# Performance work log

Measured on AMD Instinct MI355X. Metric: run time of the kernel, lower is better.

The kernel has to match this reference:

```python
import jax, jax.numpy as jnp
from jax import lax
import numpy as np

NUM_GRIDS = (40, 36, 24, 16, 12)
B, C = 4, 256
SMPL_OUT, CATE_OUT = 157, 1  # 24*6 pose + 10 shape + 3 cam; num_classes-1
SIZES = ((200, 200), (100, 100), (50, 50), (25, 25), (13, 13))


def setup_inputs():
    key = jax.random.key(0)
    ks = jax.random.split(key, 16)
    inp = {}
    for i, (h, w) in enumerate(SIZES):
        inp['feat%d' % i] = jax.random.normal(ks[i], (B, C, h, w), jnp.float32)
    def W(k, shape):
        return jax.random.normal(k, shape, jnp.float32) * 0.02
    inp['smpl_w0'] = W(ks[5], (C, C + 2, 3, 3)); inp['smpl_b0'] = jnp.zeros((C,), jnp.float32)
    inp['smpl_w'] = W(ks[6], (3, C, C, 3, 3)); inp['smpl_b'] = jnp.zeros((3, C), jnp.float32)
    inp['cate_w0'] = W(ks[7], (C, C, 3, 3)); inp['cate_b0'] = jnp.zeros((C,), jnp.float32)
    inp['cate_w'] = W(ks[8], (3, C, C, 3, 3)); inp['cate_b'] = jnp.zeros((3, C), jnp.float32)
    inp['cate_head_w'] = W(ks[9], (CATE_OUT, C, 3, 3)); inp['cate_head_b'] = jnp.zeros((CATE_OUT,), jnp.float32)
    inp['smpl_head_w'] = W(ks[10], (SMPL_OUT, C, 1, 1)); inp['smpl_head_b'] = jnp.zeros((SMPL_OUT,), jnp.float32)
    inp['smpl_init'] = W(ks[11], (SMPL_OUT,))  # stands in for init_contrep/shape/cam buffer
    return inp


def conv2d(x, w, b, pad):
    y = lax.conv_general_dilated(x, w, (1, 1), [(pad, pad), (pad, pad)],
                                 dimension_numbers=('NCHW', 'OIHW', 'NCHW'))
    return y + b[None, :, None, None]


def resize_ac(x, oh, ow):
    # bilinear resize, align_corners=True (matches F.interpolate(..., align_corners=True))
    H, W = x.shape[-2], x.shape[-1]
    ys = jnp.linspace(0.0, H - 1.0, oh)
    xs = jnp.linspace(0.0, W - 1.0, ow)
    y0 = jnp.floor(ys).astype(jnp.int32); y1 = jnp.minimum(y0 + 1, H - 1)
    x0 = jnp.floor(xs).astype(jnp.int32); x1 = jnp.minimum(x0 + 1, W - 1)
    wy = (ys - y0)[:, None]; wx = xs - x0
    r0, r1 = x[..., y0, :], x[..., y1, :]
    top = r0[..., x0] * (1 - wx) + r0[..., x1] * wx
    bot = r1[..., x0] * (1 - wx) + r1[..., x1] * wx
    return top * (1 - wy) + bot * wy


def points_nms(heat):
    # max_pool2d(kernel=2, stride=1, pad=1) -> (H+1, W+1); compare on [:-1, :-1]
    hmax = lax.reduce_window(heat, -jnp.inf, lax.max, (1, 1, 2, 2), (1, 1, 1, 1),
                             [(0, 0), (0, 0), (1, 1), (1, 1)])[:, :, :-1, :-1]
    return heat * (hmax == heat).astype(heat.dtype)


def _forward(feats, p):
    # split_feats: downsample P2 by 0.5, upsample P6 to P5 size (both align_corners bilinear)
    f0 = resize_ac(feats[0], feats[0].shape[-2] // 2, feats[0].shape[-1] // 2)
    f4 = resize_ac(feats[4], feats[3].shape[-2], feats[3].shape[-1])
    new_feats = (f0, feats[1], feats[2], feats[3], f4)
    smpl_outs, cate_outs = [], []
    for idx, x in enumerate(new_feats):
        g = NUM_GRIDS[idx]
        b, _, h, w = x.shape
        xr = jnp.linspace(-1.0, 1.0, w); yr = jnp.linspace(-1.0, 1.0, h)
        yy, xx = jnp.meshgrid(yr, xr, indexing='ij')
        coord = jnp.broadcast_to(jnp.stack([xx, yy])[None], (b, 2, h, w))  # CoordConv
        smpl_feat = resize_ac(jnp.concatenate([x, coord], axis=1), g, g)
        cate_feat = resize_ac(x, g, g)
        smpl_feat = jax.nn.relu(conv2d(smpl_feat, p['smpl_w0'], p['smpl_b0'], 1))
        cate_feat = jax.nn.relu(conv2d(cate_feat, p['cate_w0'], p['cate_b0'], 1))
        for i in range(3):  # remaining stacked convs (weights shared across levels)
            smpl_feat = jax.nn.relu(conv2d(smpl_feat, p['smpl_w'][i], p['smpl_b'][i], 1))
            cate_feat = jax.nn.relu(conv2d(cate_feat, p['cate_w'][i], p['cate_b'][i], 1))
        cate_pred = conv2d(cate_feat, p['cate_head_w'], p['cate_head_b'], 1)
        smpl_pred = conv2d(smpl_feat, p['smpl_head_w'], p['smpl_head_b'], 0) \
                    + p['smpl_init'][None, :, None, None]
        # eval=True branch: points-NMS on sigmoid heatmap, NHWC permute
        cate_pred = points_nms(jax.nn.sigmoid(cate_pred)).transpose(0, 2, 3, 1)
        smpl_pred = smpl_pred.transpose(0, 2, 3, 1)
        smpl_outs.append(smpl_pred); cate_outs.append(cate_pred)
    return tuple(smpl_outs) + tuple(cate_outs)


def reference(feat0, feat1, feat2, feat3, feat4, smpl_w0, smpl_b0, smpl_w, smpl_b,
              cate_w0, cate_b0, cate_w, cate_b, cate_head_w, cate_head_b,
              smpl_head_w, smpl_head_b, smpl_init):
    p = dict(smpl_w0=smpl_w0, smpl_b0=smpl_b0, smpl_w=smpl_w, smpl_b=smpl_b,
             cate_w0=cate_w0, cate_b0=cate_b0, cate_w=cate_w, cate_b=cate_b,
             cate_head_w=cate_head_w, cate_head_b=cate_head_b,
             smpl_head_w=smpl_head_w, smpl_head_b=smpl_head_b, smpl_init=smpl_init)
    return _forward((feat0, feat1, feat2, feat3, feat4), p)
```

## Files before the change

kernel.cpp:

```cpp
#include <hip/hip_runtime.h>
#include <math.h>
#include <stdint.h>

#define NLEV 5
#define PPT 17616
#define HPX 320

typedef __attribute__((ext_vector_type(8))) __bf16 bf16x8;
typedef __attribute__((ext_vector_type(4))) float f32x4;
typedef unsigned int u32;
typedef unsigned short u16;

#define MFMA16 __builtin_amdgcn_mfma_f32_16x16x32_bf16

__device__ __forceinline__ u32 f2bf(float f) {
  u32 u = __builtin_bit_cast(u32, f);
  return (u + 0x7FFFu + ((u >> 16) & 1u)) >> 16;
}
__device__ __forceinline__ u32 packSplit(float v) {
  u32 hi = f2bf(v);
  float fhi = __builtin_bit_cast(float, hi << 16);
  u32 lo = f2bf(v - fhi);
  return hi | (lo << 16);
}
__device__ __forceinline__ float unpackSum(u32 w) {
  return __builtin_bit_cast(float, w << 16) +
         __builtin_bit_cast(float, w & 0xFFFF0000u);
}
__device__ __forceinline__ void splitPerm(const uint4& a, const uint4& b, uint4& hq,
                                          uint4& lq) {
  hq.x = __builtin_amdgcn_perm(a.y, a.x, 0x05040100u);
  hq.y = __builtin_amdgcn_perm(a.w, a.z, 0x05040100u);
  hq.z = __builtin_amdgcn_perm(b.y, b.x, 0x05040100u);
  hq.w = __builtin_amdgcn_perm(b.w, b.z, 0x05040100u);
  lq.x = __builtin_amdgcn_perm(a.y, a.x, 0x07060302u);
  lq.y = __builtin_amdgcn_perm(a.w, a.z, 0x07060302u);
  lq.z = __builtin_amdgcn_perm(b.y, b.x, 0x07060302u);
  lq.w = __builtin_amdgcn_perm(b.w, b.z, 0x07060302u);
}


struct PrepDesc {
  const float* src[9];
  int Cin[9];
  int Cout[9];
  int CB[9];
  int TAPS[9];
  int nCoT[9];
  int dstOff[9];
};

__global__ __launch_bounds__(256) void prep_weights(PrepDesc pd, u16* __restrict__ wHi,
                                                    u16* __restrict__ wLo) {
  int cfg = blockIdx.y;
  int CB = pd.CB[cfg];
  int TAPS = pd.TAPS[cfg];
  int KS = CB * TAPS;
  int total = KS * 2048 * pd.nCoT[cfg];
  int didx = blockIdx.x * 256 + threadIdx.x;
  if (didx >= total) return;
  int j = didx & 7;
  int lane = (didx >> 3) & 63;
  int wco = (didx >> 9) & 1;
  int f = (didx >> 10) & 1;
  int rest = didx >> 11;
  int ks = rest % KS;
  int coT = rest / KS;
  int cb = ks / TAPS;
  int tap = ks - cb * TAPS;
  int ci = cb * 32 + ((lane >> 4) << 3) + j;
  int co = coT * 64 + wco * 32 + f * 16 + (lane & 15);
  float v = 0.f;
  if (ci < pd.Cin[cfg] && co < pd.Cout[cfg])
    v = pd.src[cfg][((size_t)co * pd.Cin[cfg] + ci) * TAPS + tap];
  u32 hi = f2bf(v);
  float fhi = __builtin_bit_cast(float, hi << 16);
  u32 lo = f2bf(v - fhi);
  wHi[pd.dstOff[cfg] + didx] = (u16)hi;
  wLo[pd.dstOff[cfg] + didx] = (u16)lo;
}

struct ZeroDesc {
  int padOff[NLEV];
  int g[NLEV];
};

__global__ __launch_bounds__(256) void halo_zero(u32* __restrict__ base, ZeroDesc zd) {
  int px = blockIdx.x * 256 + threadIdx.x;
  if (px >= PPT) return;
  int l = 0;
#pragma unroll
  for (int i = 1; i < NLEV; i++)
    if (px >= zd.padOff[i]) l = i;
  int g = zd.g[l], gp2 = g + 2, hp2 = gp2 * gp2;
  int local = px - zd.padOff[l];
  int b = local / hp2;
  int rem = local - b * hp2;
  int yy = rem / gp2, xx = rem - yy * gp2;
  if (yy >= 1 && yy <= g && xx >= 1 && xx <= g) return;
  int r = blockIdx.y;
  uint4 z = {0u, 0u, 0u, 0u};
  u32* p = base + ((size_t)r * PPT + px) * 8;
  *(uint4*)p = z;
  *(uint4*)(p + 4) = z;
}

struct BuildDesc {
  const float* src[NLEV];
  int H[NLEV];
  int mid[NLEV];
  int P[NLEV];
  int g[NLEV];
  int padOff[NLEV];
};

__device__ __forceinline__ float bsample(const float* __restrict__ pl, int H, int W,
                                         float fy, float fx) {
  int y0 = (int)floorf(fy);
  int y1 = min(y0 + 1, H - 1);
  float wy = fy - (float)y0;
  int x0 = (int)floorf(fx);
  int x1 = min(x0 + 1, W - 1);
  float wx = fx - (float)x0;
  const float* r0 = pl + (size_t)y0 * W;
  const float* r1 = pl + (size_t)y1 * W;
  float top = r0[x0] * (1.f - wx) + r0[x1] * wx;
  float bot = r1[x0] * (1.f - wx) + r1[x1] * wx;
  return top * (1.f - wy) + bot * wy;
}

__global__ __launch_bounds__(256) void build_all(BuildDesc bd, u32* __restrict__ dst) {
  int l = blockIdx.y;
  int P = bd.P[l];
  int g = bd.g[l];
  int total = 258 * P;
  int idx = blockIdx.x * 256 + threadIdx.x;
  if (idx >= total) return;
  int c = idx / P;
  int p = idx - c * P;
  int gg = g * g;
  int b = p / gg;
  int pr = p - b * gg;
  int i = pr / g;
  int j = pr - i * g;
  float val;
  if (c >= 256) {
    int tt = (c == 256) ? j : i;
    val = -1.f + 2.f * (float)tt / (float)(g - 1);
  } else {
    int H = bd.H[l], W = bd.H[l];
    int mid = bd.mid[l];
    const float* pl = bd.src[l] + ((size_t)b * 256 + c) * H * W;
    if (!mid) {
      float fy = (float)i * (float)(H - 1) / (float)(g - 1);
      float fx = (float)j * (float)(W - 1) / (float)(g - 1);
      val = bsample(pl, H, W, fy, fx);
    } else {
      int midh = mid, midw = mid;
      float fym = (float)i * (float)(midh - 1) / (float)(g - 1);
      float fxm = (float)j * (float)(midw - 1) / (float)(g - 1);
      int y0 = (int)floorf(fym);
      int y1 = min(y0 + 1, midh - 1);
      float wy = fym - (float)y0;
      int x0 = (int)floorf(fxm);
      int x1 = min(x0 + 1, midw - 1);
      float wx = fxm - (float)x0;
      float sy0 = (float)y0 * (float)(H - 1) / (float)(midh - 1);
      float sy1 = (float)y1 * (float)(H - 1) / (float)(midh - 1);
      float sx0 = (float)x0 * (float)(W - 1) / (float)(midw - 1);
      float sx1 = (float)x1 * (float)(W - 1) / (float)(midw - 1);
      float v00 = bsample(pl, H, W, sy0, sx0);
      float v01 = bsample(pl, H, W, sy0, sx1);
      float v10 = bsample(pl, H, W, sy1, sx0);
      float v11 = bsample(pl, H, W, sy1, sx1);
      float top = v00 * (1.f - wx) + v01 * wx;
      float bot = v10 * (1.f - wx) + v11 * wx;
      val = top * (1.f - wy) + bot * wy;
    }
  }
  int gp2 = g + 2;
  int hpos = bd.padOff[l] + b * gp2 * gp2 + (i + 1) * gp2 + (j + 1);
  dst[((size_t)(c >> 3) * PPT + hpos) * 8 + (c & 7)] = packSplit(val);
}

struct ConvDesc {
  int tS[NLEV + 1];
  int padOff[NLEV];
  int g[NLEV];
  int P[NLEV];
};

__global__ __launch_bounds__(256) void conv_mfma(
    const u32* __restrict__ inS, const u32* __restrict__ inC,
    const u16* __restrict__ wHiB, const u16* __restrict__ wLoB, int wOffS,
    int wOffC, const float* __restrict__ bS, const float* __restrict__ bC,
    u32* __restrict__ outS, u32* __restrict__ outC, ConvDesc d, int CBS, int CBC) {
  const int bid = blockIdx.x;
  const int xcd = bid & 7;
  const int i6 = bid >> 3;
  const int tower = i6 & 1;
  const int coT = (i6 >> 1) & 3;
  const int tile = xcd + (i6 >> 3) * 8;
  if (tile >= d.tS[NLEV]) return;

  const u32* __restrict__ actIn = tower ? inC : inS;
  u32* __restrict__ actOut = tower ? outC : outS;
  const u16* __restrict__ wH = wHiB + (tower ? wOffC : wOffS);
  const u16* __restrict__ wL = wLoB + (tower ? wOffC : wOffS);
  const float* __restrict__ bias = tower ? bC : bS;
  const int CB = tower ? CBC : CBS;
  const int KS = CB * 9;

  int l = 0;
#pragma unroll
  for (int i = 1; i < NLEV; i++)
    if (tile >= d.tS[i]) l = i;
  const int g = d.g[l];
  const int gp2 = g + 2, hp2 = gp2 * gp2, gg = g * g;
  const int padOff = d.padOff[l];
  const int Pl = d.P[l];
  const int ptile = (tile - d.tS[l]) * 128;

  const int t = threadIdx.x;
  const int lane = t & 63;
  const int wv = t >> 6;
  const int wco = wv & 1, wp = wv >> 1;
  const int kb = lane >> 4;
  const int sgr = wv;
  const int spx = lane;

  int h0;
  {
    int b0 = ptile / gg, pr0 = ptile - b0 * gg;
    int y0 = pr0 / g, x0 = pr0 - y0 * g;
    h0 = padOff + b0 * hp2 + (y0 + 1) * gp2 + (x0 + 1) - gp2 - 1;
  }

  int hRel[4], ob[4];
  bool vst[4];
#pragma unroll
  for (int fi = 0; fi < 4; fi++) {
    int pb = ptile + wp * 64 + fi * 16;
    vst[fi] = pb < Pl;
    int pf = pb + (lane & 15);
    if (pf >= Pl) pf = Pl - 1;
    int b = pf / gg, pr = pf - b * gg;
    int y = pr / g, x = pr - y * g;
    int h = padOff + b * hp2 + (y + 1) * gp2 + (x + 1);
    hRel[fi] = h - h0;
    ob[fi] = h;
  }

  __shared__ u32 halo[4 * 2 * HPX * 4];

  f32x4 acc[2][4];
#pragma unroll
  for (int c = 0; c < 2; c++)
#pragma unroll
    for (int fi = 0; fi < 4; fi++) acc[c][fi] = (f32x4){0.f, 0.f, 0.f, 0.f};

  const size_t wbase =
      (size_t)coT * KS * 2048 + (size_t)wco * 512 + (size_t)lane * 8;
  bf16x8 ah0 = *(const bf16x8*)(wH + wbase);
  bf16x8 ah1 = *(const bf16x8*)(wH + wbase + 1024);
  bf16x8 al0 = *(const bf16x8*)(wL + wbase);
  bf16x8 al1 = *(const bf16x8*)(wL + wbase + 1024);

  for (int cb = 0; cb < CB; ++cb) {
    __syncthreads();
    {
      const int gr = cb * 4 + sgr;
      const u32* srcp = actIn + ((size_t)gr * PPT + h0) * 8;
      u32* dhi = halo + sgr * (2 * HPX * 4);
      u32* dlo = dhi + HPX * 4;
#pragma unroll
      for (int i = 0; i < 5; i++) {
        int px = i * 64 + spx;
        uint4 a = *(const uint4*)(srcp + (size_t)px * 8);
        uint4 b2 = *(const uint4*)(srcp + (size_t)px * 8 + 4);
        uint4 hq, lq;
        splitPerm(a, b2, hq, lq);
        *(uint4*)(dhi + px * 4) = hq;
        *(uint4*)(dlo + px * 4) = lq;
      }
    }
    __syncthreads();

#pragma unroll
    for (int tap = 0; tap < 9; ++tap) {
      const int ks = cb * 9 + tap;
      bf16x8 ah0n, ah1n, al0n, al1n;
      const bool have = (ks + 1) < KS;
      if (have) {
        size_t wo = wbase + (size_t)(ks + 1) * 2048;
        ah0n = *(const bf16x8*)(wH + wo);
        ah1n = *(const bf16x8*)(wH + wo + 1024);
        al0n = *(const bf16x8*)(wL + wo);
        al1n = *(const bf16x8*)(wL + wo + 1024);
      }
      const int toff = (tap / 3 - 1) * gp2 + (tap % 3) - 1;
      const u32* kbase = halo + kb * (2 * HPX * 4);
#pragma unroll
      for (int fi = 0; fi < 4; fi++) {
        const u32* p0 = kbase + (hRel[fi] + toff) * 4;
        bf16x8 bh = __builtin_bit_cast(bf16x8, *(const uint4*)p0);
        bf16x8 bl = __builtin_bit_cast(bf16x8, *(const uint4*)(p0 + HPX * 4));
        acc[0][fi] = MFMA16(ah0, bh, acc[0][fi], 0, 0, 0);
        acc[0][fi] = MFMA16(ah0, bl, acc[0][fi], 0, 0, 0);
        acc[0][fi] = MFMA16(al0, bh, acc[0][fi], 0, 0, 0);
        acc[1][fi] = MFMA16(ah1, bh, acc[1][fi], 0, 0, 0);
        acc[1][fi] = MFMA16(ah1, bl, acc[1][fi], 0, 0, 0);
        acc[1][fi] = MFMA16(al1, bh, acc[1][fi], 0, 0, 0);
      }
      if (have) {
        ah0 = ah0n;
        ah1 = ah1n;
        al0 = al0n;
        al1 = al1n;
      }
    }
  }

  const int coBase = coT * 64 + wco * 32 + ((lane >> 4) << 2);
  float4 bA = *(const float4*)(bias + coBase);
  float4 bB = *(const float4*)(bias + coBase + 16);
  const size_t rowA = (size_t)(coBase >> 3) * PPT;
  const size_t rowB = (size_t)((coBase + 16) >> 3) * PPT;
  const int sub = coBase & 7;
#pragma unroll
  for (int fi = 0; fi < 4; fi++) {
    if (!vst[fi]) continue;
    uint4 s;
    s.x = packSplit(fmaxf(acc[0][fi][0] + bA.x, 0.f));
    s.y = packSplit(fmaxf(acc[0][fi][1] + bA.y, 0.f));
    s.z = packSplit(fmaxf(acc[0][fi][2] + bA.z, 0.f));
    s.w = packSplit(fmaxf(acc[0][fi][3] + bA.w, 0.f));
    *(uint4*)(actOut + (rowA + ob[fi]) * 8 + sub) = s;
    s.x = packSplit(fmaxf(acc[1][fi][0] + bB.x, 0.f));
    s.y = packSplit(fmaxf(acc[1][fi][1] + bB.y, 0.f));
    s.z = packSplit(fmaxf(acc[1][fi][2] + bB.z, 0.f));
    s.w = packSplit(fmaxf(acc[1][fi][3] + bB.w, 0.f));
    *(uint4*)(actOut + (rowB + ob[fi]) * 8 + sub) = s;
  }
}

struct HeadDesc {
  int tS64[NLEV + 1];
  int padOff[NLEV];
  int g[NLEV];
  int outOff[NLEV];
};

__global__ __launch_bounds__(256) void head1x1(
    const u32* __restrict__ actIn, const u16* __restrict__ wH,
    const u16* __restrict__ wL, const float* __restrict__ bias,
    const float* __restrict__ bias2, float* __restrict__ outB, HeadDesc d) {
  const int bx = blockIdx.x;
  const int coT = blockIdx.y;
  int l = 0;
#pragma unroll
  for (int i = 1; i < NLEV; i++)
    if (bx >= d.tS64[i]) l = i;
  const int g = d.g[l], gp2 = g + 2, hp2 = gp2 * gp2, gg = g * g;
  const int ptile = (bx - d.tS64[l]) * 64;
  const int t = threadIdx.x, lane = t & 63, wv = t >> 6;
  const int wco = wv & 1, wp = wv >> 1, kb = lane >> 4;

  int hp[2], pF[2];
#pragma unroll
  for (int fi = 0; fi < 2; fi++) {
    int pf = ptile + wp * 32 + fi * 16 + (lane & 15);
    pF[fi] = pf;
    int b = pf / gg, pr = pf - b * gg, y = pr / g, x = pr - y * g;
    hp[fi] = d.padOff[l] + b * hp2 + (y + 1) * gp2 + (x + 1);
  }
  f32x4 acc[2][2];
#pragma unroll
  for (int c = 0; c < 2; c++)
#pragma unroll
    for (int fi = 0; fi < 2; fi++) acc[c][fi] = (f32x4){0.f, 0.f, 0.f, 0.f};

  const size_t wbase = (size_t)coT * 8 * 2048 + (size_t)wco * 512 + (size_t)lane * 8;
  for (int cb = 0; cb < 8; ++cb) {
    size_t wo = wbase + (size_t)cb * 2048;
    bf16x8 ah0 = *(const bf16x8*)(wH + wo);
    bf16x8 ah1 = *(const bf16x8*)(wH + wo + 1024);
    bf16x8 al0 = *(const bf16x8*)(wL + wo);
    bf16x8 al1 = *(const bf16x8*)(wL + wo + 1024);
    const int gr = cb * 4 + kb;
#pragma unroll
    for (int fi = 0; fi < 2; fi++) {
      const u32* bp = actIn + ((size_t)gr * PPT + hp[fi]) * 8;
      uint4 a = *(const uint4*)bp;
      uint4 b2 = *(const uint4*)(bp + 4);
      uint4 hq, lq;
      splitPerm(a, b2, hq, lq);
      bf16x8 bh = __builtin_bit_cast(bf16x8, hq);
      bf16x8 bl = __builtin_bit_cast(bf16x8, lq);
      acc[0][fi] = MFMA16(ah0, bh, acc[0][fi], 0, 0, 0);
      acc[0][fi] = MFMA16(ah0, bl, acc[0][fi], 0, 0, 0);
      acc[0][fi] = MFMA16(al0, bh, acc[0][fi], 0, 0, 0);
      acc[1][fi] = MFMA16(ah1, bh, acc[1][fi], 0, 0, 0);
      acc[1][fi] = MFMA16(ah1, bl, acc[1][fi], 0, 0, 0);
      acc[1][fi] = MFMA16(al1, bh, acc[1][fi], 0, 0, 0);
    }
  }
  const int coBase = coT * 64 + wco * 32 + ((lane >> 4) << 2);
#pragma unroll
  for (int c = 0; c < 2; c++)
#pragma unroll
    for (int fi = 0; fi < 2; fi++)
#pragma unroll
      for (int i = 0; i < 4; i++) {
        int co = coBase + c * 16 + i;
        if (co < 157)
          outB[d.outOff[l] + (size_t)pF[fi] * 157 + co] =
              acc[c][fi][i] + bias[co] + bias2[co];
      }
}

struct CHDesc {
  int tS64[NLEV + 1];
  int padOff[NLEV];
  int g[NLEV];
  int outOff[NLEV];
};

__global__ __launch_bounds__(256) void cate_head_all(
    const u32* __restrict__ actIn, const float* __restrict__ w,
    const float* __restrict__ bias, float* __restrict__ heat, CHDesc d) {
  int tile = blockIdx.x;
  int l = 0;
#pragma unroll
  for (int i = 1; i < NLEV; i++)
    if (tile >= d.tS64[i]) l = i;
  const int g = d.g[l];
  const int gp2 = g + 2, hp2 = gp2 * gp2, gg = g * g;
  const int t = threadIdx.x;
  const int ps = t & 63;
  const int cw = t >> 6;
  const int ptile = (tile - d.tS64[l]) * 64;
  int p = ptile + ps;
  int b = p / gg, pr = p - b * gg, y = pr / g, x = pr - y * g;
  const int hbase = d.padOff[l] + b * hp2 + (y + 1) * gp2 + (x + 1);

  __shared__ float ws[32][9][8];
  for (int i = t; i < 2304; i += 256) {
    int ci = i / 9, tap = i - ci * 9;
    ws[ci >> 3][tap][ci & 7] = w[i];
  }
  __syncthreads();

  float s = 0.f;
  for (int gr = cw; gr < 32; gr += 4) {
    const u32* bp = actIn + ((size_t)gr * PPT + hbase) * 8;
#pragma unroll
    for (int tap = 0; tap < 9; tap++) {
      const int toff = (tap / 3 - 1) * gp2 + (tap % 3) - 1;
      uint4 q0 = *(const uint4*)(bp + (ptrdiff_t)toff * 8);
      uint4 q1 = *(const uint4*)(bp + (ptrdiff_t)toff * 8 + 4);
      const float* wp = ws[gr][tap];
      s += unpackSum(q0.x) * wp[0] + unpackSum(q0.y) * wp[1] +
           unpackSum(q0.z) * wp[2] + unpackSum(q0.w) * wp[3] +
           unpackSum(q1.x) * wp[4] + unpackSum(q1.y) * wp[5] +
           unpackSum(q1.z) * wp[6] + unpackSum(q1.w) * wp[7];
    }
  }
  __shared__ float red[4][64];
  red[cw][ps] = s;
  __syncthreads();
  if (cw == 0) {
    float tot = bias[0] + red[0][ps] + red[1][ps] + red[2][ps] + red[3][ps];
    heat[d.outOff[l] + p] = 1.f / (1.f + expf(-tot));
  }
}

struct SmallDesc {
  int P[NLEV];
  int g[NLEV];
  int inOff[NLEV];
  int outOff[NLEV];
};

__global__ void nms_all(const float* __restrict__ heat, float* __restrict__ out,
                        SmallDesc d) {
  int l = blockIdx.y;
  int P = d.P[l], g = d.g[l];
  int gg = g * g;
  int p = blockIdx.x * 256 + threadIdx.x;
  if (p >= P) return;
  int pr = p % gg;
  int y = pr / g;
  int x = pr - y * g;
  const float* hb = heat + d.inOff[l];
  float c = hb[p], m = c;
  if (y > 0) {
    m = fmaxf(m, hb[p - g]);
    if (x > 0) m = fmaxf(m, hb[p - g - 1]);
  }
  if (x > 0) m = fmaxf(m, hb[p - 1]);
  out[d.outOff[l] + p] = (m == c) ? c : 0.f;
}

extern "C" void kernel_launch(void* const* d_in, const int* in_sizes, int n_in,
                              void* d_out, int out_size, void* d_ws, size_t ws_size,
                              hipStream_t stream) {
  const float* feat[5];
  for (int i = 0; i < 5; i++) feat[i] = (const float*)d_in[i];
  const float* smpl_w0 = (const float*)d_in[5];
  const float* smpl_b0 = (const float*)d_in[6];
  const float* smpl_w = (const float*)d_in[7];
  const float* smpl_b = (const float*)d_in[8];
  const float* cate_w0 = (const float*)d_in[9];
  const float* cate_b0 = (const float*)d_in[10];
  const float* cate_w = (const float*)d_in[11];
  const float* cate_b = (const float*)d_in[12];
  const float* cate_head_w = (const float*)d_in[13];
  const float* cate_head_b = (const float*)d_in[14];
  const float* smpl_head_w = (const float*)d_in[15];
  const float* smpl_head_b = (const float*)d_in[16];
  const float* smpl_init = (const float*)d_in[17];
  float* out = (float*)d_out;

  static const int GR[5] = {40, 36, 24, 16, 12};
  static const int SH[5] = {200, 100, 50, 25, 13};
  static const int MIDW[5] = {100, 0, 0, 0, 25};

  int P[5], cumP[6], tS64[6], tS128[6], padOff[5];
  cumP[0] = 0;
  tS64[0] = 0;
  tS128[0] = 0;
  int po = 0;
  for (int l = 0; l < 5; l++) {
    P[l] = 4 * GR[l] * GR[l];
    cumP[l + 1] = cumP[l] + P[l];
    tS64[l + 1] = tS64[l] + P[l] / 64;
    tS128[l + 1] = tS128[l] + (P[l] + 127) / 128;
    padOff[l] = po;
    po += 4 * (GR[l] + 2) * (GR[l] + 2);
  }

  int smpl_off[5], cate_off[5];
  {
    int off = 0;
    for (int l = 0; l < 5; l++) {
      smpl_off[l] = off;
      off += P[l] * 157;
    }
    for (int l = 0; l < 5; l++) {
      cate_off[l] = off;
      off += P[l];
    }
  }

  u32* bufA = (u32*)d_ws;
  u32* bufBs = bufA + (size_t)36 * PPT * 8;
  u32* bufCs = bufBs + (size_t)32 * PPT * 8;
  u32* bufBc = bufCs + (size_t)32 * PPT * 8;
  u32* bufCc = bufBc + (size_t)32 * PPT * 8;
  float* heat = (float*)(bufCc + (size_t)32 * PPT * 8);
  u16* wHi = (u16*)(heat + 15488);

  PrepDesc pd;
  const size_t LSTR = (size_t)256 * 256 * 9;
  pd.src[0] = smpl_w0;
  pd.src[1] = smpl_w;
  pd.src[2] = smpl_w + LSTR;
  pd.src[3] = smpl_w + 2 * LSTR;
  pd.src[4] = cate_w0;
  pd.src[5] = cate_w;
  pd.src[6] = cate_w + LSTR;
  pd.src[7] = cate_w + 2 * LSTR;
  pd.src[8] = smpl_head_w;
  for (int i = 0; i < 9; i++) {
    pd.Cin[i] = 256;
    pd.Cout[i] = 256;
    pd.CB[i] = 8;
    pd.TAPS[i] = 9;
    pd.nCoT[i] = 4;
  }
  pd.Cin[0] = 258;
  pd.CB[0] = 9;
  pd.Cout[8] = 157;
  pd.TAPS[8] = 1;
  pd.nCoT[8] = 3;
  size_t WTOT = 0;
  for (int i = 0; i < 9; i++) {
    pd.dstOff[i] = (int)WTOT;
    WTOT += (size_t)pd.CB[i] * pd.TAPS[i] * 2048 * pd.nCoT[i];
  }
  u16* wLo = wHi + WTOT;

  hipMemsetAsync(bufA, 0, (size_t)36 * PPT * 32, stream);
  ZeroDesc zd;
  for (int l = 0; l < 5; l++) {
    zd.padOff[l] = padOff[l];
    zd.g[l] = GR[l];
  }
  hipLaunchKernelGGL(halo_zero, dim3((PPT + 255) / 256, 128), dim3(256), 0, stream,
                     bufBs, zd);

  hipLaunchKernelGGL(prep_weights, dim3(2592, 9), dim3(256), 0, stream, pd, wHi, wLo);

  BuildDesc bd;
  for (int l = 0; l < 5; l++) {
    bd.src[l] = feat[l];
    bd.H[l] = SH[l];
    bd.mid[l] = MIDW[l];
    bd.P[l] = P[l];
    bd.g[l] = GR[l];
    bd.padOff[l] = padOff[l];
  }
  hipLaunchKernelGGL(build_all, dim3((258 * P[0] + 255) / 256, 5), dim3(256), 0,
                     stream, bd, bufA);

  ConvDesc cd;
  HeadDesc hd;
  CHDesc chd;
  SmallDesc nd;
  for (int i = 0; i <= 5; i++) {
    cd.tS[i] = tS128[i];
    hd.tS64[i] = tS64[i];
    chd.tS64[i] = tS64[i];
  }
  for (int l = 0; l < 5; l++) {
    cd.padOff[l] = padOff[l];
    cd.g[l] = GR[l];
    cd.P[l] = P[l];
    hd.padOff[l] = padOff[l];
    hd.g[l] = GR[l];
    hd.outOff[l] = smpl_off[l];
    chd.padOff[l] = padOff[l];
    chd.g[l] = GR[l];
    chd.outOff[l] = cumP[l];
    nd.P[l] = P[l];
    nd.g[l] = GR[l];
    nd.inOff[l] = cumP[l];
    nd.outOff[l] = cate_off[l];
  }

  const int NT64 = tS64[5];
  const int CGRID = 8 * 128;
  hipLaunchKernelGGL(conv_mfma, dim3(CGRID), dim3(256), 0, stream, bufA, bufA, wHi,
                     wLo, pd.dstOff[0], pd.dstOff[4], smpl_b0, cate_b0, bufBs, bufBc,
                     cd, 9, 8);
  hipLaunchKernelGGL(conv_mfma, dim3(CGRID), dim3(256), 0, stream, bufBs, bufBc, wHi,
                     wLo, pd.dstOff[1], pd.dstOff[5], smpl_b + 0, cate_b + 0, bufCs,
                     bufCc, cd, 8, 8);
  hipLaunchKernelGGL(conv_mfma, dim3(CGRID), dim3(256), 0, stream, bufCs, bufCc, wHi,
                     wLo, pd.dstOff[2], pd.dstOff[6], smpl_b + 256, cate_b + 256,
                     bufBs, bufBc, cd, 8, 8);
  hipLaunchKernelGGL(conv_mfma, dim3(CGRID), dim3(256), 0, stream, bufBs, bufBc, wHi,
                     wLo, pd.dstOff[3], pd.dstOff[7], smpl_b + 512, cate_b + 512,
                     bufCs, bufCc, cd, 8, 8);
  hipLaunchKernelGGL(head1x1, dim3(NT64, 3), dim3(256), 0, stream, bufCs,
                     wHi + pd.dstOff[8], wLo + pd.dstOff[8], smpl_head_b, smpl_init,
                     out, hd);
  hipLaunchKernelGGL(cate_head_all, dim3(NT64), dim3(256), 0, stream, bufCc,
                     cate_head_w, cate_head_b, heat, chd);
  hipLaunchKernelGGL(nms_all, dim3((P[0] + 255) / 256, 5), dim3(256), 0, stream, heat,
                     out, nd);
  (void)in_sizes;
  (void)n_in;
  (void)out_size;
  (void)ws_size;
}
```

Before: 528.5 us.

## Store activations as split hi/lo planes and double-buffer halo via async LDS loads

Activations were stored as interleaved packed hi/lo bf16 words that each conv block split with perm instructions while staging into shared memory. They are now stored as separate hi and lo planes, so staging can use global_load_lds direct-to-LDS copies into a double-buffered halo. The next channel block is prefetched while MFMAs run on the current one, which removes the perm work and one barrier per iteration. In exchange shared memory use doubles, which may reduce occupancy, and the epilogue now issues narrower 8-byte stores.

```diff
diff --git a/kernel.cpp b/kernel.cpp
--- a/kernel.cpp
+++ b/kernel.cpp
@@ -17,26 +17,12 @@
   u32 u = __builtin_bit_cast(u32, f);
   return (u + 0x7FFFu + ((u >> 16) & 1u)) >> 16;
 }
-__device__ __forceinline__ u32 packSplit(float v) {
-  u32 hi = f2bf(v);
-  float fhi = __builtin_bit_cast(float, hi << 16);
-  u32 lo = f2bf(v - fhi);
-  return hi | (lo << 16);
-}
-__device__ __forceinline__ float unpackSum(u32 w) {
-  return __builtin_bit_cast(float, w << 16) +
-         __builtin_bit_cast(float, w & 0xFFFF0000u);
-}
-__device__ __forceinline__ void splitPerm(const uint4& a, const uint4& b, uint4& hq,
-                                          uint4& lq) {
-  hq.x = __builtin_amdgcn_perm(a.y, a.x, 0x05040100u);
-  hq.y = __builtin_amdgcn_perm(a.w, a.z, 0x05040100u);
-  hq.z = __builtin_amdgcn_perm(b.y, b.x, 0x05040100u);
-  hq.w = __builtin_amdgcn_perm(b.w, b.z, 0x05040100u);
-  lq.x = __builtin_amdgcn_perm(a.y, a.x, 0x07060302u);
-  lq.y = __builtin_amdgcn_perm(a.w, a.z, 0x07060302u);
-  lq.z = __builtin_amdgcn_perm(b.y, b.x, 0x07060302u);
-  lq.w = __builtin_amdgcn_perm(b.w, b.z, 0x07060302u);
+__device__ __forceinline__ void split2(float v, u32& hi, u32& lo) {
+  hi = f2bf(v);
+  lo = f2bf(v - __builtin_bit_cast(float, hi << 16));
+}
+__device__ __forceinline__ float bf2f(u32 bits16) {
+  return __builtin_bit_cast(float, bits16 << 16);
 }
 
 
@@ -73,9 +59,8 @@
   float v = 0.f;
   if (ci < pd.Cin[cfg] && co < pd.Cout[cfg])
     v = pd.src[cfg][((size_t)co * pd.Cin[cfg] + ci) * TAPS + tap];
-  u32 hi = f2bf(v);
-  float fhi = __builtin_bit_cast(float, hi << 16);
-  u32 lo = f2bf(v - fhi);
+  u32 hi, lo;
+  split2(v, hi, lo);
   wHi[pd.dstOff[cfg] + didx] = (u16)hi;
   wLo[pd.dstOff[cfg] + didx] = (u16)lo;
 }
@@ -85,7 +70,7 @@
   int g[NLEV];
 };
 
-__global__ __launch_bounds__(256) void halo_zero(u32* __restrict__ base, ZeroDesc zd) {
+__global__ __launch_bounds__(256) void halo_zero(u16* __restrict__ base, ZeroDesc zd) {
   int px = blockIdx.x * 256 + threadIdx.x;
   if (px >= PPT) return;
   int l = 0;
@@ -100,9 +85,7 @@
   if (yy >= 1 && yy <= g && xx >= 1 && xx <= g) return;
   int r = blockIdx.y;
   uint4 z = {0u, 0u, 0u, 0u};
-  u32* p = base + ((size_t)r * PPT + px) * 8;
-  *(uint4*)p = z;
-  *(uint4*)(p + 4) = z;
+  *(uint4*)(base + ((size_t)r * PPT + px) * 8) = z;
 }
 
 struct BuildDesc {
@@ -129,7 +112,7 @@
   return top * (1.f - wy) + bot * wy;
 }
 
-__global__ __launch_bounds__(256) void build_all(BuildDesc bd, u32* __restrict__ dst) {
+__global__ __launch_bounds__(256) void build_all(BuildDesc bd, u16* __restrict__ dst) {
   int l = blockIdx.y;
   int P = bd.P[l];
   int g = bd.g[l];
@@ -180,7 +163,11 @@
   }
   int gp2 = g + 2;
   int hpos = bd.padOff[l] + b * gp2 * gp2 + (i + 1) * gp2 + (j + 1);
-  dst[((size_t)(c >> 3) * PPT + hpos) * 8 + (c & 7)] = packSplit(val);
+  u32 hi, lo;
+  split2(val, hi, lo);
+  size_t base = ((size_t)(c >> 3) * PPT + hpos) * 8 + (c & 7);
+  dst[base] = (u16)hi;
+  dst[(size_t)36 * PPT * 8 + base] = (u16)lo;
 }
 
 struct ConvDesc {
@@ -191,10 +178,10 @@
 };
 
 __global__ __launch_bounds__(256) void conv_mfma(
-    const u32* __restrict__ inS, const u32* __restrict__ inC,
+    const u16* __restrict__ inS, const u16* __restrict__ inC, int inRows,
     const u16* __restrict__ wHiB, const u16* __restrict__ wLoB, int wOffS,
     int wOffC, const float* __restrict__ bS, const float* __restrict__ bC,
-    u32* __restrict__ outS, u32* __restrict__ outC, ConvDesc d, int CBS, int CBC) {
+    u16* __restrict__ outS, u16* __restrict__ outC, ConvDesc d, int CBS, int CBC) {
   const int bid = blockIdx.x;
   const int xcd = bid & 7;
   const int i6 = bid >> 3;
@@ -203,8 +190,10 @@
   const int tile = xcd + (i6 >> 3) * 8;
   if (tile >= d.tS[NLEV]) return;
 
-  const u32* __restrict__ actIn = tower ? inC : inS;
-  u32* __restrict__ actOut = tower ? outC : outS;
+  const u16* __restrict__ inHi = tower ? inC : inS;
+  const u16* __restrict__ inLo = inHi + (size_t)inRows * PPT * 8;
+  u16* __restrict__ outHi = tower ? outC : outS;
+  u16* __restrict__ outLo = outHi + (size_t)32 * PPT * 8;
   const u16* __restrict__ wH = wHiB + (tower ? wOffC : wOffS);
   const u16* __restrict__ wL = wLoB + (tower ? wOffC : wOffS);
   const float* __restrict__ bias = tower ? bC : bS;
@@ -227,7 +216,6 @@
   const int wco = wv & 1, wp = wv >> 1;
   const int kb = lane >> 4;
   const int sgr = wv;
-  const int spx = lane;
 
   int h0;
   {
@@ -251,7 +239,7 @@
     ob[fi] = h;
   }
 
-  __shared__ u32 halo[4 * 2 * HPX * 4];
+  __shared__ u16 halo[2 * 4 * 2 * HPX * 8];
 
   f32x4 acc[2][4];
 #pragma unroll
@@ -266,25 +254,31 @@
   bf16x8 al0 = *(const bf16x8*)(wL + wbase);
   bf16x8 al1 = *(const bf16x8*)(wL + wbase + 1024);
 
+#define STAGE(dbuf, cbn)                                                          \
+  {                                                                               \
+    const int gr_ = (cbn)*4 + sgr;                                                \
+    const u16* ghi_ = inHi + ((size_t)gr_ * PPT + h0) * 8;                        \
+    const u16* glo_ = inLo + ((size_t)gr_ * PPT + h0) * 8;                        \
+    u16* lb_ = halo + (size_t)(((dbuf)*4 + sgr) * 2) * (HPX * 8);                 \
+    _Pragma("unroll") for (int i_ = 0; i_ < 5; i_++) {                            \
+      __builtin_amdgcn_global_load_lds(                                           \
+          (const __attribute__((address_space(1))) void*)(ghi_ +                  \
+                                                          (size_t)(i_ * 64 + lane) * 8), \
+          (__attribute__((address_space(3))) void*)(lb_ + i_ * 64 * 8), 16, 0, 0);\
+      __builtin_amdgcn_global_load_lds(                                           \
+          (const __attribute__((address_space(1))) void*)(glo_ +                  \
+                                                          (size_t)(i_ * 64 + lane) * 8), \
+          (__attribute__((address_space(3))) void*)(lb_ + HPX * 8 + i_ * 64 * 8), \
+          16, 0, 0);                                                              \
+    }                                                                             \
+  }
+
+  STAGE(0, 0);
+
   for (int cb = 0; cb < CB; ++cb) {
+    const int cur = cb & 1;
     __syncthreads();
-    {
-      const int gr = cb * 4 + sgr;
-      const u32* srcp = actIn + ((size_t)gr * PPT + h0) * 8;
-      u32* dhi = halo + sgr * (2 * HPX * 4);
-      u32* dlo = dhi + HPX * 4;
-#pragma unroll
-      for (int i = 0; i < 5; i++) {
-        int px = i * 64 + spx;
-        uint4 a = *(const uint4*)(srcp + (size_t)px * 8);
-        uint4 b2 = *(const uint4*)(srcp + (size_t)px * 8 + 4);
-        uint4 hq, lq;
-        splitPerm(a, b2, hq, lq);
-        *(uint4*)(dhi + px * 4) = hq;
-        *(uint4*)(dlo + px * 4) = lq;
-      }
-    }
-    __syncthreads();
+    if (cb + 1 < CB) STAGE(cur ^ 1, cb + 1);
 
 #pragma unroll
     for (int tap = 0; tap < 9; ++tap) {
@@ -299,12 +293,12 @@
         al1n = *(const bf16x8*)(wL + wo + 1024);
       }
       const int toff = (tap / 3 - 1) * gp2 + (tap % 3) - 1;
-      const u32* kbase = halo + kb * (2 * HPX * 4);
+      const u16* kbase = halo + (size_t)((cur * 4 + kb) * 2) * (HPX * 8);
 #pragma unroll
       for (int fi = 0; fi < 4; fi++) {
-        const u32* p0 = kbase + (hRel[fi] + toff) * 4;
-        bf16x8 bh = __builtin_bit_cast(bf16x8, *(const uint4*)p0);
-        bf16x8 bl = __builtin_bit_cast(bf16x8, *(const uint4*)(p0 + HPX * 4));
+        const u16* p0 = kbase + (hRel[fi] + toff) * 8;
+        bf16x8 bh = *(const bf16x8*)p0;
+        bf16x8 bl = *(const bf16x8*)(p0 + HPX * 8);
         acc[0][fi] = MFMA16(ah0, bh, acc[0][fi], 0, 0, 0);
         acc[0][fi] = MFMA16(ah0, bl, acc[0][fi], 0, 0, 0);
         acc[0][fi] = MFMA16(al0, bh, acc[0][fi], 0, 0, 0);
@@ -320,27 +314,38 @@
       }
     }
   }
+#undef STAGE
 
   const int coBase = coT * 64 + wco * 32 + ((lane >> 4) << 2);
-  float4 bA = *(const float4*)(bias + coBase);
-  float4 bB = *(const float4*)(bias + coBase + 16);
+  float bAv[4], bBv[4];
+#pragma unroll
+  for (int i = 0; i < 4; i++) {
+    bAv[i] = bias[coBase + i];
+    bBv[i] = bias[coBase + 16 + i];
+  }
   const size_t rowA = (size_t)(coBase >> 3) * PPT;
   const size_t rowB = (size_t)((coBase + 16) >> 3) * PPT;
   const int sub = coBase & 7;
 #pragma unroll
   for (int fi = 0; fi < 4; fi++) {
     if (!vst[fi]) continue;
-    uint4 s;
-    s.x = packSplit(fmaxf(acc[0][fi][0] + bA.x, 0.f));
-    s.y = packSplit(fmaxf(acc[0][fi][1] + bA.y, 0.f));
-    s.z = packSplit(fmaxf(acc[0][fi][2] + bA.z, 0.f));
-    s.w = packSplit(fmaxf(acc[0][fi][3] + bA.w, 0.f));
-    *(uint4*)(actOut + (rowA + ob[fi]) * 8 + sub) = s;
-    s.x = packSplit(fmaxf(acc[1][fi][0] + bB.x, 0.f));
-    s.y = packSplit(fmaxf(acc[1][fi][1] + bB.y, 0.f));
-    s.z = packSplit(fmaxf(acc[1][fi][2] + bB.z, 0.f));
-    s.w = packSplit(fmaxf(acc[1][fi][3] + bB.w, 0.f));
-    *(uint4*)(actOut + (rowB + ob[fi]) * 8 + sub) = s;
+    u32 h[4], lo[4];
+#pragma unroll
+    for (int i = 0; i < 4; i++)
+      split2(fmaxf(acc[0][fi][i] + bAv[i], 0.f), h[i], lo[i]);
+    uint2 hs = {h[0] | (h[1] << 16), h[2] | (h[3] << 16)};
+    uint2 ls = {lo[0] | (lo[1] << 16), lo[2] | (lo[3] << 16)};
+    *(uint2*)(outHi + (rowA + ob[fi]) * 8 + sub) = hs;
+    *(uint2*)(outLo + (rowA + ob[fi]) * 8 + sub) = ls;
+#pragma unroll
+    for (int i = 0; i < 4; i++)
+      split2(fmaxf(acc[1][fi][i] + bBv[i], 0.f), h[i], lo[i]);
+    hs.x = h[0] | (h[1] << 16);
+    hs.y = h[2] | (h[3] << 16);
+    ls.x = lo[0] | (lo[1] << 16);
+    ls.y = lo[2] | (lo[3] << 16);
+    *(uint2*)(outHi + (rowB + ob[fi]) * 8 + sub) = hs;
+    *(uint2*)(outLo + (rowB + ob[fi]) * 8 + sub) = ls;
   }
 }
 
@@ -352,9 +357,10 @@
 };
 
 __global__ __launch_bounds__(256) void head1x1(
-    const u32* __restrict__ actIn, const u16* __restrict__ wH,
-    const u16* __restrict__ wL, const float* __restrict__ bias,
-    const float* __restrict__ bias2, float* __restrict__ outB, HeadDesc d) {
+    const u16* __restrict__ inHi, const u16* __restrict__ inLo,
+    const u16* __restrict__ wH, const u16* __restrict__ wL,
+    const float* __restrict__ bias, const float* __restrict__ bias2,
+    float* __restrict__ outB, HeadDesc d) {
   const int bx = blockIdx.x;
   const int coT = blockIdx.y;
   int l = 0;
@@ -390,13 +396,8 @@
     const int gr = cb * 4 + kb;
 #pragma unroll
     for (int fi = 0; fi < 2; fi++) {
-      const u32* bp = actIn + ((size_t)gr * PPT + hp[fi]) * 8;
-      uint4 a = *(const uint4*)bp;
-      uint4 b2 = *(const uint4*)(bp + 4);
-      uint4 hq, lq;
-      splitPerm(a, b2, hq, lq);
-      bf16x8 bh = __builtin_bit_cast(bf16x8, hq);
-      bf16x8 bl = __builtin_bit_cast(bf16x8, lq);
+      bf16x8 bh = *(const bf16x8*)(inHi + ((size_t)gr * PPT + hp[fi]) * 8);
+      bf16x8 bl = *(const bf16x8*)(inLo + ((size_t)gr * PPT + hp[fi]) * 8);
       acc[0][fi] = MFMA16(ah0, bh, acc[0][fi], 0, 0, 0);
       acc[0][fi] = MFMA16(ah0, bl, acc[0][fi], 0, 0, 0);
       acc[0][fi] = MFMA16(al0, bh, acc[0][fi], 0, 0, 0);
@@ -427,8 +428,9 @@
 };
 
 __global__ __launch_bounds__(256) void cate_head_all(
-    const u32* __restrict__ actIn, const float* __restrict__ w,
-    const float* __restrict__ bias, float* __restrict__ heat, CHDesc d) {
+    const u16* __restrict__ inHi, const u16* __restrict__ inLo,
+    const float* __restrict__ w, const float* __restrict__ bias,
+    float* __restrict__ heat, CHDesc d) {
   int tile = blockIdx.x;
   int l = 0;
 #pragma unroll
@@ -453,17 +455,22 @@
 
   float s = 0.f;
   for (int gr = cw; gr < 32; gr += 4) {
-    const u32* bp = actIn + ((size_t)gr * PPT + hbase) * 8;
+    const u16* ph = inHi + ((size_t)gr * PPT + hbase) * 8;
+    const u16* pl = inLo + ((size_t)gr * PPT + hbase) * 8;
 #pragma unroll
     for (int tap = 0; tap < 9; tap++) {
       const int toff = (tap / 3 - 1) * gp2 + (tap % 3) - 1;
-      uint4 q0 = *(const uint4*)(bp + (ptrdiff_t)toff * 8);
-      uint4 q1 = *(const uint4*)(bp + (ptrdiff_t)toff * 8 + 4);
+      uint4 hq = *(const uint4*)(ph + (ptrdiff_t)toff * 8);
+      uint4 lq = *(const uint4*)(pl + (ptrdiff_t)toff * 8);
       const float* wp = ws[gr][tap];
-      s += unpackSum(q0.x) * wp[0] + unpackSum(q0.y) * wp[1] +
-           unpackSum(q0.z) * wp[2] + unpackSum(q0.w) * wp[3] +
-           unpackSum(q1.x) * wp[4] + unpackSum(q1.y) * wp[5] +
-           unpackSum(q1.z) * wp[6] + unpackSum(q1.w) * wp[7];
+      s += (bf2f(hq.x & 0xFFFFu) + bf2f(lq.x & 0xFFFFu)) * wp[0] +
+           (bf2f(hq.x >> 16) + bf2f(lq.x >> 16)) * wp[1] +
+           (bf2f(hq.y & 0xFFFFu) + bf2f(lq.y & 0xFFFFu)) * wp[2] +
+           (bf2f(hq.y >> 16) + bf2f(lq.y >> 16)) * wp[3] +
+           (bf2f(hq.z & 0xFFFFu) + bf2f(lq.z & 0xFFFFu)) * wp[4] +
+           (bf2f(hq.z >> 16) + bf2f(lq.z >> 16)) * wp[5] +
+           (bf2f(hq.w & 0xFFFFu) + bf2f(lq.w & 0xFFFFu)) * wp[6] +
+           (bf2f(hq.w >> 16) + bf2f(lq.w >> 16)) * wp[7];
     }
   }
   __shared__ float red[4][64];
@@ -553,12 +560,12 @@
     }
   }
 
-  u32* bufA = (u32*)d_ws;
-  u32* bufBs = bufA + (size_t)36 * PPT * 8;
-  u32* bufCs = bufBs + (size_t)32 * PPT * 8;
-  u32* bufBc = bufCs + (size_t)32 * PPT * 8;
-  u32* bufCc = bufBc + (size_t)32 * PPT * 8;
-  float* heat = (float*)(bufCc + (size_t)32 * PPT * 8);
+  u16* bufA = (u16*)d_ws;
+  u16* bufBs = bufA + (size_t)72 * PPT * 8;
+  u16* bufCs = bufBs + (size_t)64 * PPT * 8;
+  u16* bufBc = bufCs + (size_t)64 * PPT * 8;
+  u16* bufCc = bufBc + (size_t)64 * PPT * 8;
+  float* heat = (float*)(bufCc + (size_t)64 * PPT * 8);
   u16* wHi = (u16*)(heat + 15488);
 
   PrepDesc pd;
@@ -597,7 +604,7 @@
     zd.padOff[l] = padOff[l];
     zd.g[l] = GR[l];
   }
-  hipLaunchKernelGGL(halo_zero, dim3((PPT + 255) / 256, 128), dim3(256), 0, stream,
+  hipLaunchKernelGGL(halo_zero, dim3((PPT + 255) / 256, 256), dim3(256), 0, stream,
                      bufBs, zd);
 
   hipLaunchKernelGGL(prep_weights, dim3(2592, 9), dim3(256), 0, stream, pd, wHi, wLo);
@@ -641,25 +648,26 @@
 
   const int NT64 = tS64[5];
   const int CGRID = 8 * 128;
-  hipLaunchKernelGGL(conv_mfma, dim3(CGRID), dim3(256), 0, stream, bufA, bufA, wHi,
-                     wLo, pd.dstOff[0], pd.dstOff[4], smpl_b0, cate_b0, bufBs, bufBc,
-                     cd, 9, 8);
-  hipLaunchKernelGGL(conv_mfma, dim3(CGRID), dim3(256), 0, stream, bufBs, bufBc, wHi,
-                     wLo, pd.dstOff[1], pd.dstOff[5], smpl_b + 0, cate_b + 0, bufCs,
-                     bufCc, cd, 8, 8);
-  hipLaunchKernelGGL(conv_mfma, dim3(CGRID), dim3(256), 0, stream, bufCs, bufCc, wHi,
-                     wLo, pd.dstOff[2], pd.dstOff[6], smpl_b + 256, cate_b + 256,
-                     bufBs, bufBc, cd, 8, 8);
-  hipLaunchKernelGGL(conv_mfma, dim3(CGRID), dim3(256), 0, stream, bufBs, bufBc, wHi,
-                     wLo, pd.dstOff[3], pd.dstOff[7], smpl_b + 512, cate_b + 512,
+  hipLaunchKernelGGL(conv_mfma, dim3(CGRID), dim3(256), 0, stream, bufA, bufA, 36,
+                     wHi, wLo, pd.dstOff[0], pd.dstOff[4], smpl_b0, cate_b0, bufBs,
+                     bufBc, cd, 9, 8);
+  hipLaunchKernelGGL(conv_mfma, dim3(CGRID), dim3(256), 0, stream, bufBs, bufBc, 32,
+                     wHi, wLo, pd.dstOff[1], pd.dstOff[5], smpl_b + 0, cate_b + 0,
                      bufCs, bufCc, cd, 8, 8);
+  hipLaunchKernelGGL(conv_mfma, dim3(CGRID), dim3(256), 0, stream, bufCs, bufCc, 32,
+                     wHi, wLo, pd.dstOff[2], pd.dstOff[6], smpl_b + 256,
+                     cate_b + 256, bufBs, bufBc, cd, 8, 8);
+  hipLaunchKernelGGL(conv_mfma, dim3(CGRID), dim3(256), 0, stream, bufBs, bufBc, 32,
+                     wHi, wLo, pd.dstOff[3], pd.dstOff[7], smpl_b + 512,
+                     cate_b + 512, bufCs, bufCc, cd, 8, 8);
   hipLaunchKernelGGL(head1x1, dim3(NT64, 3), dim3(256), 0, stream, bufCs,
-                     wHi + pd.dstOff[8], wLo + pd.dstOff[8], smpl_head_b, smpl_init,
-                     out, hd);
+                     bufCs + (size_t)32 * PPT * 8, wHi + pd.dstOff[8],
+                     wLo + pd.dstOff[8], smpl_head_b, smpl_init, out, hd);
   hipLaunchKernelGGL(cate_head_all, dim3(NT64), dim3(256), 0, stream, bufCc,
-                     cate_head_w, cate_head_b, heat, chd);
-  hipLaunchKernelGGL(nms_all, dim3((P[0] + 255) / 256, 5), dim3(256), 0, stream, heat,
-                     out, nd);
+                     bufCc + (size_t)32 * PPT * 8, cate_head_w, cate_head_b, heat,
+                     chd);
+  hipLaunchKernelGGL(nms_all, dim3((P[0] + 255) / 256, 5), dim3(256), 0, stream,
+                     heat, out, nd);
   (void)in_sizes;
   (void)n_in;
   (void)out_size;
```

Result: faster. 506.9 us (-4.1%).
